# Optimization experiments

Hardware: AMD Instinct MI355X
Metric: run time of the kernel (lower is better)

Reference implementation:

```python
import jax, jax.numpy as jnp
import numpy as np

FP8_E4M3_MAX = 448.0

def fp8_quant_dequant(t):
    """Per-tensor symmetric fp8 e4m3 quantize -> dequantize (simulated fp8)."""
    amax = jnp.max(jnp.abs(t))
    scale = FP8_E4M3_MAX / jnp.maximum(amax, 1e-12)
    q = (t * scale).astype(jnp.float8_e4m3fn).astype(t.dtype) / scale
    return q

def setup_inputs() -> dict:
    key = jax.random.key(0)
    kx, kw = jax.random.split(key)
    N, IN, OUT = 8192, 4096, 4096
    x = jax.random.normal(kx, (N, IN), dtype=jnp.float32)
    weight = jax.random.normal(kw, (IN, OUT), dtype=jnp.float32)
    bias = jnp.zeros((OUT,), dtype=jnp.float32)
    return {"x": x, "weight": weight, "bias": bias}

def reference(x, weight, bias):
    # FP8LinearFunction: quantize activations and weights to fp8 e4m3 with
    # per-tensor scaling, GEMM, dequantize, fused bias add.
    qx = fp8_quant_dequant(x)          # [N, in]
    qw = fp8_quant_dequant(weight)     # [in, out]  (weight stored untransposed)
    return jnp.matmul(qx, qw) + bias   # [N, out]
```

## Files before the change

### kernel.cpp

```cpp
#include <hip/hip_runtime.h>
#include <stdint.h>

#define M_DIM 8192
#define K_DIM 4096
#define N_DIM 4096
#define FP8_MAX 448.0f

typedef float floatx4 __attribute__((ext_vector_type(4)));



__device__ __forceinline__ uint32_t pack4_fp8(float a, float b, float c, float d) {
    int v = __builtin_amdgcn_cvt_pk_fp8_f32(a, b, 0, false);
    v = __builtin_amdgcn_cvt_pk_fp8_f32(c, d, v, true);
    return (uint32_t)v;
}

__device__ __forceinline__ void gload_lds16(const uint8_t* g, uint8_t* l) {
    __builtin_amdgcn_global_load_lds(
        (const __attribute__((address_space(1))) uint32_t*)g,
        (__attribute__((address_space(3))) uint32_t*)l,
        16, 0, 0);
}

__device__ __forceinline__ float scale_from_amax(float amax) {
    return FP8_MAX / fmaxf(amax, 1e-12f);
}


__global__ void init_amax_kernel(uint32_t* amax) {
    amax[0] = 0u;
    amax[1] = 0u;
}


__global__ void amax_kernel(const float* __restrict__ src, long n, uint32_t* out_bits) {
    long i = (long)blockIdx.x * blockDim.x + threadIdx.x;
    long stride = (long)gridDim.x * blockDim.x;
    const float4* s4 = (const float4*)src;
    long n4 = n >> 2;
    float m = 0.0f;
    for (long j = i; j < n4; j += stride) {
        float4 v = s4[j];
        m = fmaxf(m, fmaxf(fmaxf(fabsf(v.x), fabsf(v.y)), fmaxf(fabsf(v.z), fabsf(v.w))));
    }
    #pragma unroll
    for (int off = 32; off > 0; off >>= 1)
        m = fmaxf(m, __shfl_down(m, off, 64));
    __shared__ float smax[4];
    int wave = threadIdx.x >> 6;
    if ((threadIdx.x & 63) == 0) smax[wave] = m;
    __syncthreads();
    if (threadIdx.x == 0) {
        float bm = fmaxf(fmaxf(smax[0], smax[1]), fmaxf(smax[2], smax[3]));
        atomicMax(out_bits, __float_as_uint(bm));
    }
}


__global__ __launch_bounds__(256)
void quantX_kernel(const float* __restrict__ x, uint8_t* __restrict__ qx,
                   const uint32_t* __restrict__ amax_bits) {
    float scale = scale_from_amax(__uint_as_float(*amax_bits));
    long tileM = (long)blockIdx.y * 128;
    int kb = blockIdx.x * 64;
    uint8_t* outT = qx + ((size_t)blockIdx.y * (K_DIM / 64) + blockIdx.x) * 8192;
    int t = threadIdx.x;
    #pragma unroll
    for (int it = 0; it < 4; ++it) {
        int G = t + it * 256;
        int g = G >> 7;
        int rr = G & 127;
        const float4* p = (const float4*)(x + (tileM + rr) * K_DIM + kb + g * 8);
        float4 a = p[0];
        float4 b = p[1];
        uint2 o;
        o.x = pack4_fp8(a.x * scale, a.y * scale, a.z * scale, a.w * scale);
        o.y = pack4_fp8(b.x * scale, b.y * scale, b.z * scale, b.w * scale);
        *(uint2*)(outT + (size_t)G * 8) = o;
    }
}


__global__ __launch_bounds__(256)
void quantW_kernel(const float* __restrict__ w, uint8_t* __restrict__ qwT,
                   const uint32_t* __restrict__ amax_bits) {
    float scale = scale_from_amax(__uint_as_float(*amax_bits));
    int n0 = blockIdx.y * 128;
    int kb = blockIdx.x * 64;
    uint8_t* outT = qwT + ((size_t)blockIdx.y * (K_DIM / 64) + blockIdx.x) * 8192;
    int t = threadIdx.x;
    #pragma unroll
    for (int it = 0; it < 4; ++it) {
        int G = t + it * 256;
        int g = G >> 7;
        int rr = G & 127;
        const float* col = w + (long)(kb + g * 8) * N_DIM + n0 + rr;
        float v[8];
        #pragma unroll
        for (int j = 0; j < 8; ++j)
            v[j] = col[(long)j * N_DIM] * scale;
        uint2 o;
        o.x = pack4_fp8(v[0], v[1], v[2], v[3]);
        o.y = pack4_fp8(v[4], v[5], v[6], v[7]);
        *(uint2*)(outT + (size_t)G * 8) = o;
    }
}


#define BM 128
#define BN 128
#define BK 64

__global__ __launch_bounds__(256)
void gemm_kernel(const uint8_t* __restrict__ qx, const uint8_t* __restrict__ qwT,
                 const float* __restrict__ bias, float* __restrict__ C,
                 const uint32_t* __restrict__ amax_bits) {
    float sx = scale_from_amax(__uint_as_float(amax_bits[0]));
    float sw = scale_from_amax(__uint_as_float(amax_bits[1]));
    float dq = 1.0f / (sx * sw);

    __shared__ __align__(16) uint8_t sA[BM * BK];
    __shared__ __align__(16) uint8_t sB[BN * BK];

    int tid = threadIdx.x;
    int wave = tid >> 6;
    int lane = tid & 63;

    long tileM = (long)blockIdx.y * BM;
    long tileN = (long)blockIdx.x * BN;

    const uint8_t* gA = qx + tileM * K_DIM;
    const uint8_t* gB = qwT + tileN * K_DIM;

    floatx4 acc[4][4];
    #pragma unroll
    for (int i = 0; i < 4; ++i)
        #pragma unroll
        for (int j = 0; j < 4; ++j)
            acc[i][j] = (floatx4)0.0f;

    int waveM = (wave >> 1) * 64;
    int waveN = (wave & 1) * 64;
    int q = lane >> 4;
    int aOff = q * 1024 + (waveM + (lane & 15)) * 8;
    int bOff = q * 1024 + (waveN + (lane & 15)) * 8;

    for (int k0 = 0; k0 < K_DIM; k0 += BK) {
        __syncthreads();
        const uint8_t* tA = gA + k0 * 128;
        const uint8_t* tB = gB + k0 * 128;
        #pragma unroll
        for (int it = 0; it < 2; ++it) {
            int c = (tid + it * 256) * 16;
            gload_lds16(tA + c, sA + c);
            gload_lds16(tB + c, sB + c);
        }
        __syncthreads();

        #pragma unroll
        for (int kk = 0; kk < BK; kk += 32) {
            long aF[4], bF[4];
            #pragma unroll
            for (int mi = 0; mi < 4; ++mi)
                aF[mi] = *(const long*)(sA + aOff + kk * 128 + mi * 128);
            #pragma unroll
            for (int ni = 0; ni < 4; ++ni)
                bF[ni] = *(const long*)(sB + bOff + kk * 128 + ni * 128);
            #pragma unroll
            for (int mi = 0; mi < 4; ++mi)
                #pragma unroll
                for (int ni = 0; ni < 4; ++ni)
                    acc[mi][ni] = __builtin_amdgcn_mfma_f32_16x16x32_fp8_fp8(
                        aF[mi], bF[ni], acc[mi][ni], 0, 0, 0);
        }
    }

    long colBase = tileN + waveN + (lane & 15);
    float bV[4];
    #pragma unroll
    for (int ni = 0; ni < 4; ++ni) bV[ni] = bias[colBase + ni * 16];

    #pragma unroll
    for (int mi = 0; mi < 4; ++mi) {
        #pragma unroll
        for (int r = 0; r < 4; ++r) {
            long row = tileM + waveM + mi * 16 + (lane >> 4) * 4 + r;
            float* crow = C + row * N_DIM;
            #pragma unroll
            for (int ni = 0; ni < 4; ++ni)
                crow[colBase + ni * 16] = acc[mi][ni][r] * dq + bV[ni];
        }
    }
}


extern "C" void kernel_launch(void* const* d_in, const int* in_sizes, int n_in,
                              void* d_out, int out_size, void* d_ws, size_t ws_size,
                              hipStream_t stream) {
    const float* x = (const float*)d_in[0];
    const float* w = (const float*)d_in[1];
    const float* bias = (const float*)d_in[2];
    float* out = (float*)d_out;

    uint32_t* amax = (uint32_t*)d_ws;
    uint8_t* qx = (uint8_t*)d_ws + 256;
    uint8_t* qwT = qx + (size_t)M_DIM * K_DIM;

    init_amax_kernel<<<1, 64, 0, stream>>>(amax);
    amax_kernel<<<2048, 256, 0, stream>>>(x, (long)M_DIM * K_DIM, amax + 0);
    amax_kernel<<<2048, 256, 0, stream>>>(w, (long)K_DIM * N_DIM, amax + 1);
    quantX_kernel<<<dim3(K_DIM / 64, M_DIM / 128), 256, 0, stream>>>(x, qx, amax + 0);
    quantW_kernel<<<dim3(K_DIM / 64, N_DIM / 128), 256, 0, stream>>>(w, qwT, amax + 1);
    gemm_kernel<<<dim3(N_DIM / BN, M_DIM / BM), 256, 0, stream>>>(qx, qwT, bias, out, amax);
}
```

Baseline: 594.5 us.

## Switch GEMM to 32x32x64 scaled FP8 MFMA and merge prep kernels

Replaces the 16x16x32 fp8 MFMA with the gfx950 mfma_scale 32x32x64 f8f6f4 instruction using unit block scales. The quantize kernels now write a new tile layout so each lane can load 16-byte fragments from LDS. The two amax launches are merged into one, and the two quantize launches likewise, to cut launch overhead. The aim is higher matrix-core throughput and fewer, wider LDS reads per K step. The risk is a wrong fragment layout or scale encoding, which would give incorrect output.

```diff
diff --git a/kernel.cpp b/kernel.cpp
--- a/kernel.cpp
+++ b/kernel.cpp
@@ -6,7 +6,8 @@
 #define N_DIM 4096
 #define FP8_MAX 448.0f
 
-typedef float floatx4 __attribute__((ext_vector_type(4)));
+typedef float floatx16 __attribute__((ext_vector_type(16)));
+typedef int intx8 __attribute__((ext_vector_type(8)));
 
 
 
@@ -34,11 +35,17 @@
 }
 
 
-__global__ void amax_kernel(const float* __restrict__ src, long n, uint32_t* out_bits) {
-    long i = (long)blockIdx.x * blockDim.x + threadIdx.x;
-    long stride = (long)gridDim.x * blockDim.x;
+__global__ __launch_bounds__(256)
+void amax_kernel(const float* __restrict__ x, const float* __restrict__ w,
+                 uint32_t* __restrict__ out_bits) {
+    bool isX = blockIdx.x < 2048;
+    const float* src = isX ? x : w;
+    long n4 = (isX ? (long)M_DIM * K_DIM : (long)K_DIM * N_DIM) >> 2;
+    int bid = isX ? blockIdx.x : blockIdx.x - 2048;
+    int nb = isX ? 2048 : 1024;
+    long i = (long)bid * blockDim.x + threadIdx.x;
+    long stride = (long)nb * blockDim.x;
     const float4* s4 = (const float4*)src;
-    long n4 = n >> 2;
     float m = 0.0f;
     for (long j = i; j < n4; j += stride) {
         float4 v = s4[j];
@@ -53,57 +60,61 @@
     __syncthreads();
     if (threadIdx.x == 0) {
         float bm = fmaxf(fmaxf(smax[0], smax[1]), fmaxf(smax[2], smax[3]));
-        atomicMax(out_bits, __float_as_uint(bm));
+        atomicMax(out_bits + (isX ? 0 : 1), __float_as_uint(bm));
     }
 }
 
 
 __global__ __launch_bounds__(256)
-void quantX_kernel(const float* __restrict__ x, uint8_t* __restrict__ qx,
-                   const uint32_t* __restrict__ amax_bits) {
-    float scale = scale_from_amax(__uint_as_float(*amax_bits));
-    long tileM = (long)blockIdx.y * 128;
-    int kb = blockIdx.x * 64;
-    uint8_t* outT = qx + ((size_t)blockIdx.y * (K_DIM / 64) + blockIdx.x) * 8192;
-    int t = threadIdx.x;
-    #pragma unroll
-    for (int it = 0; it < 4; ++it) {
-        int G = t + it * 256;
-        int g = G >> 7;
-        int rr = G & 127;
-        const float4* p = (const float4*)(x + (tileM + rr) * K_DIM + kb + g * 8);
-        float4 a = p[0];
-        float4 b = p[1];
-        uint2 o;
-        o.x = pack4_fp8(a.x * scale, a.y * scale, a.z * scale, a.w * scale);
-        o.y = pack4_fp8(b.x * scale, b.y * scale, b.z * scale, b.w * scale);
-        *(uint2*)(outT + (size_t)G * 8) = o;
-    }
-}
-
-
-__global__ __launch_bounds__(256)
-void quantW_kernel(const float* __restrict__ w, uint8_t* __restrict__ qwT,
-                   const uint32_t* __restrict__ amax_bits) {
-    float scale = scale_from_amax(__uint_as_float(*amax_bits));
-    int n0 = blockIdx.y * 128;
-    int kb = blockIdx.x * 64;
-    uint8_t* outT = qwT + ((size_t)blockIdx.y * (K_DIM / 64) + blockIdx.x) * 8192;
-    int t = threadIdx.x;
-    #pragma unroll
-    for (int it = 0; it < 4; ++it) {
-        int G = t + it * 256;
-        int g = G >> 7;
-        int rr = G & 127;
-        const float* col = w + (long)(kb + g * 8) * N_DIM + n0 + rr;
-        float v[8];
-        #pragma unroll
-        for (int j = 0; j < 8; ++j)
-            v[j] = col[(long)j * N_DIM] * scale;
-        uint2 o;
-        o.x = pack4_fp8(v[0], v[1], v[2], v[3]);
-        o.y = pack4_fp8(v[4], v[5], v[6], v[7]);
-        *(uint2*)(outT + (size_t)G * 8) = o;
+void quant_kernel(const float* __restrict__ x, const float* __restrict__ w,
+                  uint8_t* __restrict__ qx, uint8_t* __restrict__ qwT,
+                  const uint32_t* __restrict__ amax_bits) {
+    int b = blockIdx.x;
+    if (b < 4096) {
+        float scale = scale_from_amax(__uint_as_float(amax_bits[0]));
+        int iy = b >> 6, ib = b & 63;
+        const float* src = x + (long)iy * 128 * K_DIM;
+        uint8_t* outT = qx + (size_t)b * 8192;
+        int kb = ib * 64;
+        #pragma unroll
+        for (int it = 0; it < 2; ++it) {
+            int G = threadIdx.x + it * 256;
+            int kq = G >> 8, rem = G & 255;
+            int mi = rem >> 6, h = (rem >> 5) & 1, r5 = rem & 31;
+            const float4* p = (const float4*)(src + (long)(mi * 32 + r5) * K_DIM
+                                              + kb + h * 32 + kq * 16);
+            float4 v0 = p[0], v1 = p[1], v2 = p[2], v3 = p[3];
+            uint4 o;
+            o.x = pack4_fp8(v0.x * scale, v0.y * scale, v0.z * scale, v0.w * scale);
+            o.y = pack4_fp8(v1.x * scale, v1.y * scale, v1.z * scale, v1.w * scale);
+            o.z = pack4_fp8(v2.x * scale, v2.y * scale, v2.z * scale, v2.w * scale);
+            o.w = pack4_fp8(v3.x * scale, v3.y * scale, v3.z * scale, v3.w * scale);
+            *(uint4*)(outT + (size_t)G * 16) = o;
+        }
+    } else {
+        float scale = scale_from_amax(__uint_as_float(amax_bits[1]));
+        b -= 4096;
+        int iy = b >> 6, ib = b & 63;
+        int n0 = iy * 128, kb = ib * 64;
+        uint8_t* outT = qwT + (size_t)b * 8192;
+        #pragma unroll
+        for (int it = 0; it < 2; ++it) {
+            int G = threadIdx.x + it * 256;
+            int kq = G >> 8, rem = G & 255;
+            int mi = rem >> 6, h = (rem >> 5) & 1, r5 = rem & 31;
+            int n = n0 + mi * 32 + r5;
+            const float* col = w + (long)(kb + h * 32 + kq * 16) * N_DIM + n;
+            float v[16];
+            #pragma unroll
+            for (int j = 0; j < 16; ++j)
+                v[j] = col[(long)j * N_DIM] * scale;
+            uint4 o;
+            o.x = pack4_fp8(v[0], v[1], v[2], v[3]);
+            o.y = pack4_fp8(v[4], v[5], v[6], v[7]);
+            o.z = pack4_fp8(v[8], v[9], v[10], v[11]);
+            o.w = pack4_fp8(v[12], v[13], v[14], v[15]);
+            *(uint4*)(outT + (size_t)G * 16) = o;
+        }
     }
 }
 
@@ -111,6 +122,7 @@
 #define BM 128
 #define BN 128
 #define BK 64
+#define UNIT_SCALE 0x7F7F7F7F
 
 __global__ __launch_bounds__(256)
 void gemm_kernel(const uint8_t* __restrict__ qx, const uint8_t* __restrict__ qwT,
@@ -126,6 +138,8 @@
     int tid = threadIdx.x;
     int wave = tid >> 6;
     int lane = tid & 63;
+    int wm = wave >> 1;
+    int wn = wave & 1;
 
     long tileM = (long)blockIdx.y * BM;
     long tileN = (long)blockIdx.x * BN;
@@ -133,18 +147,14 @@
     const uint8_t* gA = qx + tileM * K_DIM;
     const uint8_t* gB = qwT + tileN * K_DIM;
 
-    floatx4 acc[4][4];
+    floatx16 acc[2][2];
     #pragma unroll
-    for (int i = 0; i < 4; ++i)
-        #pragma unroll
-        for (int j = 0; j < 4; ++j)
-            acc[i][j] = (floatx4)0.0f;
-
-    int waveM = (wave >> 1) * 64;
-    int waveN = (wave & 1) * 64;
-    int q = lane >> 4;
-    int aOff = q * 1024 + (waveM + (lane & 15)) * 8;
-    int bOff = q * 1024 + (waveN + (lane & 15)) * 8;
+    for (int i = 0; i < 2; ++i)
+        #pragma unroll
+        for (int j = 0; j < 2; ++j)
+            acc[i][j] = (floatx16)0.0f;
+
+    int l16 = lane * 16;
 
     for (int k0 = 0; k0 < K_DIM; k0 += BK) {
         __syncthreads();
@@ -158,38 +168,45 @@
         }
         __syncthreads();
 
-        #pragma unroll
-        for (int kk = 0; kk < BK; kk += 32) {
-            long aF[4], bF[4];
+        union Frag { intx8 v; int4 q[2]; };
+        Frag fa[2], fb[2];
+        #pragma unroll
+        for (int mi = 0; mi < 2; ++mi) {
+            int ab = ((wm * 2 + mi) << 10) + l16;
+            fa[mi].q[0] = *(const int4*)(sA + ab);
+            fa[mi].q[1] = *(const int4*)(sA + 4096 + ab);
+            int bb = ((wn * 2 + mi) << 10) + l16;
+            fb[mi].q[0] = *(const int4*)(sB + bb);
+            fb[mi].q[1] = *(const int4*)(sB + 4096 + bb);
+        }
+        #pragma unroll
+        for (int mi = 0; mi < 2; ++mi)
             #pragma unroll
-            for (int mi = 0; mi < 4; ++mi)
-                aF[mi] = *(const long*)(sA + aOff + kk * 128 + mi * 128);
+            for (int ni = 0; ni < 2; ++ni)
+                acc[mi][ni] = __builtin_amdgcn_mfma_scale_f32_32x32x64_f8f6f4(
+                    fa[mi].v, fb[ni].v, acc[mi][ni],
+                    0, 0,
+                    0, UNIT_SCALE,
+                    0, UNIT_SCALE);
+    }
+
+    int cn = lane & 31;
+    int h4 = (lane >> 5) * 4;
+    #pragma unroll
+    for (int ni = 0; ni < 2; ++ni) {
+        long col = tileN + wn * 64 + ni * 32 + cn;
+        float bv = bias[col];
+        #pragma unroll
+        for (int mi = 0; mi < 2; ++mi) {
+            long rowBase = tileM + wm * 64 + mi * 32 + h4;
+            floatx16 a = acc[mi][ni];
             #pragma unroll
-            for (int ni = 0; ni < 4; ++ni)
-                bF[ni] = *(const long*)(sB + bOff + kk * 128 + ni * 128);
-            #pragma unroll
-            for (int mi = 0; mi < 4; ++mi)
+            for (int rg = 0; rg < 4; ++rg) {
+                long row = rowBase + 8 * rg;
                 #pragma unroll
-                for (int ni = 0; ni < 4; ++ni)
-                    acc[mi][ni] = __builtin_amdgcn_mfma_f32_16x16x32_fp8_fp8(
-                        aF[mi], bF[ni], acc[mi][ni], 0, 0, 0);
-        }
-    }
-
-    long colBase = tileN + waveN + (lane & 15);
-    float bV[4];
-    #pragma unroll
-    for (int ni = 0; ni < 4; ++ni) bV[ni] = bias[colBase + ni * 16];
-
-    #pragma unroll
-    for (int mi = 0; mi < 4; ++mi) {
-        #pragma unroll
-        for (int r = 0; r < 4; ++r) {
-            long row = tileM + waveM + mi * 16 + (lane >> 4) * 4 + r;
-            float* crow = C + row * N_DIM;
-            #pragma unroll
-            for (int ni = 0; ni < 4; ++ni)
-                crow[colBase + ni * 16] = acc[mi][ni][r] * dq + bV[ni];
+                for (int rr = 0; rr < 4; ++rr)
+                    C[(row + rr) * N_DIM + col] = a[rg * 4 + rr] * dq + bv;
+            }
         }
     }
 }
@@ -208,9 +225,7 @@
     uint8_t* qwT = qx + (size_t)M_DIM * K_DIM;
 
     init_amax_kernel<<<1, 64, 0, stream>>>(amax);
-    amax_kernel<<<2048, 256, 0, stream>>>(x, (long)M_DIM * K_DIM, amax + 0);
-    amax_kernel<<<2048, 256, 0, stream>>>(w, (long)K_DIM * N_DIM, amax + 1);
-    quantX_kernel<<<dim3(K_DIM / 64, M_DIM / 128), 256, 0, stream>>>(x, qx, amax + 0);
-    quantW_kernel<<<dim3(K_DIM / 64, N_DIM / 128), 256, 0, stream>>>(w, qwT, amax + 1);
+    amax_kernel<<<3072, 256, 0, stream>>>(x, w, amax);
+    quant_kernel<<<6144, 256, 0, stream>>>(x, w, qx, qwT, amax);
     gemm_kernel<<<dim3(N_DIM / BN, M_DIM / BM), 256, 0, stream>>>(qx, qwT, bias, out, amax);
 }
```

New measurement: 505.9 us. -14.9%, faster.
